# Performance work log

Hardware: AMD Instinct MI355X
Metric: run time of the kernel (lower is better)

Reference implementation:

```python
import jax, jax.numpy as jnp
import numpy as np

DEPTH = 18                 # tree levels (complete binary tree, heap layout)
N = 2**DEPTH - 1           # 262143 nodes
X_SIZE = 128
H_SIZE = 128
VOCAB = 32000


def setup_inputs() -> dict:
    key = jax.random.key(0)
    ks = jax.random.split(key, 8)
    g = lambda k, shp, sc: jax.random.normal(k, shp, dtype=jnp.float32) * sc
    return {
        "x": jax.random.randint(ks[0], (N,), 0, VOCAB, dtype=jnp.int32),
        "mask": jax.random.randint(ks[1], (N,), 0, 2, dtype=jnp.int32),
        "E": g(ks[2], (VOCAB, X_SIZE), 0.02),
        "W_iou": g(ks[3], (X_SIZE, 3 * H_SIZE), X_SIZE ** -0.5),
        "b_iou_x": jnp.zeros((3 * H_SIZE,), jnp.float32),
        "W_f": g(ks[4], (X_SIZE, H_SIZE), X_SIZE ** -0.5),
        "b_f_x": jnp.zeros((H_SIZE,), jnp.float32),
        "U_iou": g(ks[5], (H_SIZE, 3 * H_SIZE), H_SIZE ** -0.5),
        "b_iou_h": jnp.zeros((3 * H_SIZE,), jnp.float32),
        "U_f": g(ks[6], (H_SIZE, H_SIZE), H_SIZE ** -0.5),
        "b_f_h": jnp.zeros((H_SIZE,), jnp.float32),
    }


def reference(x, mask, E, W_iou, b_iou_x, W_f, b_f_x, U_iou, b_iou_h, U_f, b_f_h):
    # input_module: embedding lookup of masked token ids
    m = mask.astype(jnp.float32)[:, None]                      # [N,1]
    embeds = E[x * mask]                                       # [N,X]
    iou_in = (embeds @ W_iou + b_iou_x) * m                    # [N,3H] gated per node
    f_in = (embeds @ W_f + b_f_x) * m                          # [N,H]

    Hd = U_f.shape[0]
    h = jnp.zeros((N, Hd), jnp.float32)
    c = jnp.zeros((N, Hd), jnp.float32)

    # topological propagation: leaves -> root (prop_nodes_topo)
    for lvl in range(DEPTH - 1, -1, -1):
        s0, e0 = 2 ** lvl - 1, 2 ** (lvl + 1) - 1              # node range at this level
        iou = iou_in[s0:e0] + b_iou_h                          # apply_node bias
        if lvl == DEPTH - 1:
            c_agg = jnp.zeros((e0 - s0, Hd), jnp.float32)      # leaves: no children
        else:
            # children of node i are 2i+1 (left) and 2i+2 (right): strided gather
            hl, hr = h[2 * s0 + 1:2 * e0:2], h[2 * s0 + 2:2 * e0 + 1:2]
            cl, cr = c[2 * s0 + 1:2 * e0:2], c[2 * s0 + 2:2 * e0 + 1:2]
            # per-child forget gates (child-sum aggregator, shared U_f)
            fl = jax.nn.sigmoid(f_in[s0:e0] + hl @ U_f + b_f_h)
            fr = jax.nn.sigmoid(f_in[s0:e0] + hr @ U_f + b_f_h)
            c_agg = fl * cl + fr * cr
            iou = iou + (hl + hr) @ U_iou
        i, o, u = jnp.split(iou, 3, axis=-1)
        c_new = jax.nn.sigmoid(i) * jnp.tanh(u) + c_agg
        h_new = jax.nn.sigmoid(o) * jnp.tanh(c_new)
        h = h.at[s0:e0].set(h_new)                             # scatter back to parents
        c = c.at[s0:e0].set(c_new)
    return h                                                   # output_module = identity
```

## Files before the change

kernel.cpp:

```cpp
#include <hip/hip_runtime.h>
#include <math.h>

typedef unsigned short u16;
typedef unsigned int u32;
typedef float f32x4 __attribute__((ext_vector_type(4)));
typedef short bfrag __attribute__((ext_vector_type(8)));

#define HS 128
#define DPLANE 4096000
#define DHB    33554304

__device__ __forceinline__ float sigf(float x) { return 1.0f / (1.0f + __expf(-x)); }
__device__ __forceinline__ float tanhfast(float x) {
    float e = __expf(2.0f * x);
    return 1.0f - 2.0f / (e + 1.0f);
}
__device__ __forceinline__ u16 f2bf(float f) {
    u32 u = __float_as_uint(f);
    return (u16)((u + 0x7FFFu + ((u >> 16) & 1u)) >> 16);
}
__device__ __forceinline__ float bf2f(u16 h) { return __uint_as_float(((u32)h) << 16); }

template<int N> __device__ __forceinline__ void waitv() {
    asm volatile("s_waitcnt vmcnt(%0)" :: "i"(N) : "memory");
}

__device__ __forceinline__ float bval_int(int k, int col,
    const float* W_iou, const float* W_f, const float* U_iou, const float* U_f)
{
    if (col < 384) {
        if (k < 128) return W_iou[k * 384 + col];
        if (k < 256) return U_iou[(k - 128) * 384 + col];
        return U_iou[(k - 256) * 384 + col];
    } else if (col < 512) {
        int cc = col - 384;
        if (k < 128) return W_f[k * 128 + cc];
        if (k < 256) return U_f[(k - 128) * 128 + cc];
        return 0.0f;
    } else {
        int cc = col - 512;
        if (k < 128) return W_f[k * 128 + cc];
        if (k < 256) return 0.0f;
        return U_f[(k - 256) * 128 + cc];
    }
}

#define TOT_INT (12 * 40 * 2 * 512)
#define TOT_LEAF (4 * 24 * 2 * 512)
#define ZBF_OFF (TOT_INT + TOT_LEAF)
#define EPL_OFF (ZBF_OFF + 128)
#define TOT_E 4096000
#define ZBP_OFF (EPL_OFF + TOT_E)
#define PREP_ALL (ZBP_OFF + 128)

__global__ __launch_bounds__(256) void prep_kernel(
    const float* __restrict__ W_iou, const float* __restrict__ W_f,
    const float* __restrict__ U_iou, const float* __restrict__ U_f,
    const float* __restrict__ E,
    u16* __restrict__ Bint, u16* __restrict__ Bleaf,
    u16* __restrict__ EH, u16* __restrict__ EL,
    u16* __restrict__ zbp, float* __restrict__ zbf)
{
    int idx = blockIdx.x * 256 + threadIdx.x;
    if (idx < TOT_INT) {
        int j8 = idx & 7, l = (idx >> 3) & 63, half = (idx >> 9) & 1;
        int rest = idx >> 10;
        int cfabs = rest % 40, kc = rest / 40;
        int wq = cfabs / 5, g = cfabs % 5;
        int j = 16 * wq + (l & 15);
        int origcol = (g < 3) ? g * 128 + j : ((g == 3) ? 384 + j : 512 + j);
        int k = kc * 32 + (l >> 4) * 8 + j8;
        float v = bval_int(k, origcol, W_iou, W_f, U_iou, U_f);
        u16 hi = f2bf(v);
        Bint[idx] = half ? f2bf(v - bf2f(hi)) : hi;
    } else if (idx < TOT_INT + TOT_LEAF) {
        int i2 = idx - TOT_INT;
        int j8 = i2 & 7, l = (i2 >> 3) & 63, half = (i2 >> 9) & 1;
        int rest = i2 >> 10;
        int cfabs = rest % 24, kc = rest / 24;
        int wq = cfabs / 3, g = cfabs % 3;
        int origcol = g * 128 + 16 * wq + (l & 15);
        int k = kc * 32 + (l >> 4) * 8 + j8;
        float v = W_iou[k * 384 + origcol];
        u16 hi = f2bf(v);
        Bleaf[i2] = half ? f2bf(v - bf2f(hi)) : hi;
    } else if (idx < EPL_OFF) {
        zbf[idx - ZBF_OFF] = 0.0f;
    } else if (idx < ZBP_OFF) {
        int i3 = idx - EPL_OFF;
        float v = E[i3];
        u16 hi = f2bf(v);
        EH[i3] = hi;
        EL[i3] = f2bf(v - bf2f(hi));
    } else if (idx < PREP_ALL) {
        zbp[idx - ZBP_OFF] = 0;
    }
}

template<int NKC, int NCFA, int NCF, int MODE>
__device__ __forceinline__ void phase_gemm(
    f32x4 (&acc)[4][NCF],
    const int* __restrict__ x, const int* __restrict__ mask,
    const u16* __restrict__ EH, const u16* __restrict__ zbp,
    const u16* __restrict__ hbH,
    const u16* __restrict__ Bg,
    u16* ldsA, const u16* ldsP,
    int n0, int lastn, int t)
{
    constexpr int NB = 2 * NCF;
    const int l = t & 63, wq = t >> 6;
    const int lr = l & 15, lg = l >> 4;

    const u16 *ebp, *hb1p = nullptr, *hb2p = nullptr;
    {
        const int prow = t & 63, pk8 = ((t >> 6) & 3) * 8, pp = t >> 8;
        int ns = n0 + prow; if (ns >= lastn) ns = n0;
        const u16* Ep = pp ? (EH + DPLANE) : EH;
        ebp = (mask[ns] ? Ep + (size_t)x[ns] * HS : zbp) + pk8;
        if (MODE == 1) {
            const u16* hbp = pp ? (hbH + DHB) : hbH;
            hb1p = hbp + (size_t)(2 * ns + 1) * HS + pk8;
            hb2p = hbp + (size_t)(2 * ns + 2) * HS + pk8;
        }
    }
    auto stageA = [&](int kc, int buf) {
        const u16* src;
        if (MODE == 1) {
            int seg = kc >> 2, ks = kc & 3;
            src = (seg == 0 ? ebp : (seg == 1 ? hb1p : hb2p)) + ks * 32;
        } else {
            src = ebp + (kc & 3) * 32;
        }
        __builtin_amdgcn_global_load_lds(
            (const __attribute__((address_space(1))) void*)src,
            (__attribute__((address_space(3))) void*)(ldsA + buf * 4096 + t * 8), 16, 0, 0);
    };
    const u16* bbase = Bg + (size_t)(wq * NCF) * 1024 + (size_t)l * 8;
    auto loadB = [&](int kc, bfrag (&bh)[NCF], bfrag (&bl)[NCF]) {
        const u16* bp = bbase + (size_t)kc * ((size_t)NCFA * 1024);
#pragma unroll
        for (int cf = 0; cf < NCF; ++cf) {
            bh[cf] = *(const bfrag*)(bp + (size_t)cf * 1024);
            bl[cf] = *(const bfrag*)(bp + (size_t)cf * 1024 + 512);
        }
    };
    auto compute = [&](int kk, bfrag (&bh)[NCF], bfrag (&bl)[NCF]) {
        bfrag ah[4], al[4];
        if (MODE == 2 && kk >= 4) {
            const int seg = (kk - 4) >> 2;
            const int kk8 = ((kk - 4) & 3) * 4 + lg;
#pragma unroll
            for (int rf = 0; rf < 4; ++rf) {
                int arow = 16 * rf + lr;
                ah[rf] = *(const bfrag*)(ldsP + ((size_t)kk8 * 128 + seg * 64 + arow) * 8);
                al[rf] = *(const bfrag*)(ldsP + ((size_t)(16 + kk8) * 128 + seg * 64 + arow) * 8);
            }
        } else {
            const u16* ab = ldsA + (kk % 3) * 4096;
#pragma unroll
            for (int rf = 0; rf < 4; ++rf) {
                int arow = 16 * rf + lr;
                ah[rf] = *(const bfrag*)(ab + ((size_t)lg * 64 + arow) * 8);
                al[rf] = *(const bfrag*)(ab + ((size_t)(4 + lg) * 64 + arow) * 8);
            }
        }
#pragma unroll
        for (int cf = 0; cf < NCF; ++cf) {
#pragma unroll
            for (int rf = 0; rf < 4; ++rf)
                acc[rf][cf] = __builtin_amdgcn_mfma_f32_16x16x32_bf16(ah[rf], bh[cf], acc[rf][cf], 0, 0, 0);
#pragma unroll
            for (int rf = 0; rf < 4; ++rf)
                acc[rf][cf] = __builtin_amdgcn_mfma_f32_16x16x32_bf16(al[rf], bh[cf], acc[rf][cf], 0, 0, 0);
#pragma unroll
            for (int rf = 0; rf < 4; ++rf)
                acc[rf][cf] = __builtin_amdgcn_mfma_f32_16x16x32_bf16(ah[rf], bl[cf], acc[rf][cf], 0, 0, 0);
        }
    };

    bfrag bhA[NCF], blA[NCF], bhB[NCF], blB[NCF];
    stageA(0, 0);
    loadB(0, bhA, blA);
    stageA(1, 1);

#pragma unroll 1
    for (int kc = 0; kc < NKC; kc += 2) {
        loadB(kc + 1, bhB, blB);
        if constexpr (MODE == 2) { if (kc <= 2) waitv<NB + 1>(); else waitv<NB>(); }
        else waitv<NB + 1>();
        __builtin_amdgcn_s_barrier();
        asm volatile("" ::: "memory");
        if constexpr (MODE == 2) { if (kc + 2 < 4) stageA(kc + 2, (kc + 2) % 3); }
        else                     { if (kc + 2 <= NKC - 1) stageA(kc + 2, (kc + 2) % 3); }
        compute(kc, bhA, blA);

        { int kn = kc + 2; if (kn > NKC - 1) kn = NKC - 1; loadB(kn, bhA, blA); }
        if constexpr (MODE == 2) { if (kc == 0) waitv<NB + 1>(); else waitv<NB>(); }
        else { if (kc == NKC - 2) waitv<NB>(); else waitv<NB + 1>(); }
        __builtin_amdgcn_s_barrier();
        asm volatile("" ::: "memory");
        if constexpr (MODE == 2) { if (kc + 3 < 4) stageA(kc + 3, (kc + 3) % 3); }
        else                     { if (kc + 3 <= NKC - 1) stageA(kc + 3, (kc + 3) % 3); }
        compute(kc + 1, bhB, blB);
    }
}

template<int NCF, bool LEAF>
__device__ __forceinline__ void child_epilogue(
    f32x4 (&acc)[4][NCF],
    const int* __restrict__ mask,
    const float* __restrict__ b_iou_x, const float* __restrict__ b_f_x,
    const float* __restrict__ b_iou_h, const float* __restrict__ b_f_h,
    float* __restrict__ h, const float* __restrict__ c,
    u16* ldsP, float* ldsC,
    int n0, int lastn, int oBase, int t)
{
    const int l = t & 63, wq = t >> 6, lr = l & 15, lg = l >> 4;
    const int j = 16 * wq + lr;
    float bix = b_iou_x[j], box = b_iou_x[HS + j], bux = b_iou_x[2 * HS + j];
    float bih = b_iou_h[j], boh = b_iou_h[HS + j], buh = b_iou_h[2 * HS + j];
    float bfx = 0.0f, bfh = 0.0f;
    if constexpr (!LEAF) { bfx = b_f_x[j]; bfh = b_f_h[j]; }
#pragma unroll
    for (int rf = 0; rf < 4; ++rf) {
#pragma unroll
        for (int r = 0; r < 4; ++r) {
            int ctr = 16 * rf + 4 * lg + r;
            int n = n0 + ctr;
            if (n >= lastn) continue;
            float m = (float)mask[n];
            float iv = acc[rf][0][r] + m * bix + bih;
            float ov = acc[rf][1][r] + m * box + boh;
            float uv = acc[rf][2][r] + m * bux + buh;
            float cn;
            if constexpr (!LEAF) {
                float fl = acc[rf][3][r] + m * bfx + bfh;
                float fr = acc[rf][4][r] + m * bfx + bfh;
                float cl = c[(size_t)(2 * n + 1) * HS + j];
                float cr = c[(size_t)(2 * n + 2) * HS + j];
                cn = sigf(iv) * tanhfast(uv) + sigf(fl) * cl + sigf(fr) * cr;
            } else {
                cn = sigf(iv) * tanhfast(uv);
            }
            float hn = sigf(ov) * tanhfast(cn);
            h[(size_t)n * HS + j] = hn;
            int o = oBase + ctr;
            int half = o & 1, slot = o >> 1;
            u16 hh = f2bf(hn);
            ldsP[((size_t)(j >> 3) * 128 + half * 64 + slot) * 8 + (j & 7)] = hh;
            ldsP[((size_t)(16 + (j >> 3)) * 128 + half * 64 + slot) * 8 + (j & 7)] = f2bf(hn - bf2f(hh));
            ldsC[o * 129 + j] = cn;
        }
    }
}

__device__ __forceinline__ void parent_epilogue(
    f32x4 (&acc)[4][5],
    const int* __restrict__ mask,
    const float* __restrict__ b_iou_x, const float* __restrict__ b_f_x,
    const float* __restrict__ b_iou_h, const float* __restrict__ b_f_h,
    float* __restrict__ h, float* __restrict__ c, u16* __restrict__ hbH,
    const float* ldsC,
    int n0, int lastn, int t)
{
    u16* hbL = hbH + DHB;
    const int l = t & 63, wq = t >> 6, lr = l & 15, lg = l >> 4;
    const int j = 16 * wq + lr;
    float bix = b_iou_x[j], box = b_iou_x[HS + j], bux = b_iou_x[2 * HS + j];
    float bih = b_iou_h[j], boh = b_iou_h[HS + j], buh = b_iou_h[2 * HS + j];
    float bfx = b_f_x[j], bfh = b_f_h[j];
#pragma unroll
    for (int rf = 0; rf < 4; ++rf) {
#pragma unroll
        for (int r = 0; r < 4; ++r) {
            int ctr = 16 * rf + 4 * lg + r;
            int n = n0 + ctr;
            if (n >= lastn) continue;
            float m = (float)mask[n];
            float iv = acc[rf][0][r] + m * bix + bih;
            float ov = acc[rf][1][r] + m * box + boh;
            float uv = acc[rf][2][r] + m * bux + buh;
            float fl = acc[rf][3][r] + m * bfx + bfh;
            float fr = acc[rf][4][r] + m * bfx + bfh;
            float cl = ldsC[(2 * ctr) * 129 + j];
            float cr = ldsC[(2 * ctr + 1) * 129 + j];
            float cn = sigf(iv) * tanhfast(uv) + sigf(fl) * cl + sigf(fr) * cr;
            float hn = sigf(ov) * tanhfast(cn);
            c[(size_t)n * HS + j] = cn;
            h[(size_t)n * HS + j] = hn;
            u16 hh = f2bf(hn);
            hbH[(size_t)n * HS + j] = hh;
            hbL[(size_t)n * HS + j] = f2bf(hn - bf2f(hh));
        }
    }
}

__device__ __forceinline__ void tail_epilogue(
    f32x4 (&acc)[4][5],
    const int* __restrict__ mask,
    const float* __restrict__ b_iou_x, const float* __restrict__ b_f_x,
    const float* __restrict__ b_iou_h, const float* __restrict__ b_f_h,
    float* __restrict__ h, float* __restrict__ c, u16* __restrict__ hbH,
    int n0, int lastn, int t)
{
    u16* hbL = hbH + DHB;
    const int l = t & 63, wq = t >> 6, lr = l & 15, lg = l >> 4;
    const int j = 16 * wq + lr;
    float bix = b_iou_x[j], box = b_iou_x[HS + j], bux = b_iou_x[2 * HS + j];
    float bih = b_iou_h[j], boh = b_iou_h[HS + j], buh = b_iou_h[2 * HS + j];
    float bfx = b_f_x[j], bfh = b_f_h[j];
#pragma unroll
    for (int rf = 0; rf < 4; ++rf) {
#pragma unroll
        for (int r = 0; r < 4; ++r) {
            int ctr = 16 * rf + 4 * lg + r;
            int n = n0 + ctr;
            if (n >= lastn) continue;
            float m = (float)mask[n];
            float iv = acc[rf][0][r] + m * bix + bih;
            float ov = acc[rf][1][r] + m * box + boh;
            float uv = acc[rf][2][r] + m * bux + buh;
            float fl = acc[rf][3][r] + m * bfx + bfh;
            float fr = acc[rf][4][r] + m * bfx + bfh;
            float cl = c[(size_t)(2 * n + 1) * HS + j];
            float cr = c[(size_t)(2 * n + 2) * HS + j];
            float cn = sigf(iv) * tanhfast(uv) + sigf(fl) * cl + sigf(fr) * cr;
            float hn = sigf(ov) * tanhfast(cn);
            c[(size_t)n * HS + j] = cn;
            h[(size_t)n * HS + j] = hn;
            u16 hh = f2bf(hn);
            hbH[(size_t)n * HS + j] = hh;
            hbL[(size_t)n * HS + j] = f2bf(hn - bf2f(hh));
        }
    }
}

template<bool LEAFCH>
__global__ __launch_bounds__(512, 2) void fused_pair(
    const int* __restrict__ x, const int* __restrict__ mask,
    const u16* __restrict__ EH, const u16* __restrict__ zbp,
    const u16* __restrict__ Bint, const u16* __restrict__ Bleaf,
    const float* __restrict__ b_iou_x, const float* __restrict__ b_f_x,
    const float* __restrict__ b_iou_h, const float* __restrict__ b_f_h,
    float* __restrict__ h, float* __restrict__ c, u16* __restrict__ hbH,
    int s0p, int Mp)
{
    __shared__ __align__(16) u16 ldsA[3 * 4096];
    __shared__ __align__(16) u16 ldsP[2 * 16 * 128 * 8];
    __shared__ __align__(16) float ldsC[128 * 129];
    const int t = threadIdx.x;
    const int p0 = s0p + blockIdx.x * 64;
    const int lastp = s0p + Mp;
    const int lastc = 2 * lastp + 1;

    constexpr int CNCF = LEAFCH ? 3 : 5;
    const f32x4 zzz = {0.0f, 0.0f, 0.0f, 0.0f};

    {
        f32x4 acc[4][CNCF];
#pragma unroll
        for (int rf = 0; rf < 4; ++rf)
#pragma unroll
            for (int cf = 0; cf < CNCF; ++cf) acc[rf][cf] = zzz;
        phase_gemm<LEAFCH ? 4 : 12, LEAFCH ? 24 : 40, CNCF, LEAFCH ? 0 : 1>(
            acc, x, mask, EH, zbp, hbH, LEAFCH ? Bleaf : Bint, ldsA, ldsP, 2 * p0 + 1, lastc, t);
        child_epilogue<CNCF, LEAFCH>(acc, mask, b_iou_x, b_f_x, b_iou_h, b_f_h,
                                     h, c, ldsP, ldsC, 2 * p0 + 1, lastc, 0, t);
    }
    __syncthreads();
    {
        f32x4 acc[4][CNCF];
#pragma unroll
        for (int rf = 0; rf < 4; ++rf)
#pragma unroll
            for (int cf = 0; cf < CNCF; ++cf) acc[rf][cf] = zzz;
        phase_gemm<LEAFCH ? 4 : 12, LEAFCH ? 24 : 40, CNCF, LEAFCH ? 0 : 1>(
            acc, x, mask, EH, zbp, hbH, LEAFCH ? Bleaf : Bint, ldsA, ldsP, 2 * p0 + 65, lastc, t);
        child_epilogue<CNCF, LEAFCH>(acc, mask, b_iou_x, b_f_x, b_iou_h, b_f_h,
                                     h, c, ldsP, ldsC, 2 * p0 + 65, lastc, 64, t);
    }
    __syncthreads();
    {
        f32x4 acc[4][5];
#pragma unroll
        for (int rf = 0; rf < 4; ++rf)
#pragma unroll
            for (int cf = 0; cf < 5; ++cf) acc[rf][cf] = zzz;
        phase_gemm<12, 40, 5, 2>(acc, x, mask, EH, zbp, hbH, Bint, ldsA, ldsP, p0, lastp, t);
        parent_epilogue(acc, mask, b_iou_x, b_f_x, b_iou_h, b_f_h,
                        h, c, hbH, ldsC, p0, lastp, t);
    }
}

#define TAIL_BLOCKS 32

__device__ __forceinline__ void grid_barrier(u32* ctr, u32 target, int t) {
    __syncthreads();
    if (t == 0) {
        __threadfence();
        __hip_atomic_fetch_add(ctr, 1u, __ATOMIC_RELEASE, __HIP_MEMORY_SCOPE_AGENT);
        while (__hip_atomic_load(ctr, __ATOMIC_ACQUIRE, __HIP_MEMORY_SCOPE_AGENT) < target)
            __builtin_amdgcn_s_sleep(4);
        __threadfence();
    }
    __syncthreads();
}

__global__ __launch_bounds__(512, 2) void tail_kernel(
    const int* __restrict__ x, const int* __restrict__ mask,
    const u16* __restrict__ EH, const u16* __restrict__ zbp,
    const u16* __restrict__ Bint,
    const float* __restrict__ b_iou_x, const float* __restrict__ b_f_x,
    const float* __restrict__ b_iou_h, const float* __restrict__ b_f_h,
    float* __restrict__ h, float* __restrict__ c, u16* __restrict__ hbH,
    u32* __restrict__ bar)
{
    __shared__ __align__(16) u16 ldsA[3 * 4096];
    const int t = threadIdx.x;
    const f32x4 zzz = {0.0f, 0.0f, 0.0f, 0.0f};

#pragma unroll 1
    for (int lvl = 11; lvl >= 0; --lvl) {
        int s0 = (1 << lvl) - 1, M = 1 << lvl;
        int nb = (M + 63) >> 6;
        if ((int)blockIdx.x < nb) {
            int n0 = s0 + blockIdx.x * 64;
            int lastn = s0 + M;
            f32x4 acc[4][5];
#pragma unroll
            for (int rf = 0; rf < 4; ++rf)
#pragma unroll
                for (int cf = 0; cf < 5; ++cf) acc[rf][cf] = zzz;
            phase_gemm<12, 40, 5, 1>(acc, x, mask, EH, zbp, hbH, Bint,
                                     ldsA, nullptr, n0, lastn, t);
            tail_epilogue(acc, mask, b_iou_x, b_f_x, b_iou_h, b_f_h,
                          h, c, hbH, n0, lastn, t);
        }
        if (lvl > 0) grid_barrier(&bar[11 - lvl], TAIL_BLOCKS, t);
    }
}

extern "C" void kernel_launch(void* const* d_in, const int* in_sizes, int n_in,
                              void* d_out, int out_size, void* d_ws, size_t ws_size,
                              hipStream_t stream)
{
    const int*   x       = (const int*)d_in[0];
    const int*   mask    = (const int*)d_in[1];
    const float* E       = (const float*)d_in[2];
    const float* W_iou   = (const float*)d_in[3];
    const float* b_iou_x = (const float*)d_in[4];
    const float* W_f     = (const float*)d_in[5];
    const float* b_f_x   = (const float*)d_in[6];
    const float* U_iou   = (const float*)d_in[7];
    const float* b_iou_h = (const float*)d_in[8];
    const float* U_f     = (const float*)d_in[9];
    const float* b_f_h   = (const float*)d_in[10];

    float* h = (float*)d_out;
    char* ws = (char*)d_ws;

    u16*   Bint  = (u16*)(ws);
    u16*   Bleaf = (u16*)(ws + 983040);
    float* zbf   = (float*)(ws + 1179648);
    u32*   bar   = (u32*)(ws + 1179648);
    u16*   EH    = (u16*)(ws + 1180160);
    u16*   EL    = (u16*)(ws + 9372160);
    u16*   zbp   = (u16*)(ws + 17564160);
    float* c     = (float*)(ws + 17564416);
    u16*   hbH   = (u16*)(ws + 151781632);

    prep_kernel<<<PREP_ALL / 256, 256, 0, stream>>>(
        W_iou, W_f, U_iou, U_f, E, Bint, Bleaf, EH, EL, zbp, zbf);

    for (int lvl = 16; lvl >= 12; lvl -= 2) {
        int s0p = (1 << lvl) - 1, Mp = 1 << lvl;
        int blocks = (Mp + 63) / 64;
        if (lvl == 16)
            fused_pair<true><<<blocks, 512, 0, stream>>>(
                x, mask, EH, zbp, Bint, Bleaf,
                b_iou_x, b_f_x, b_iou_h, b_f_h, h, c, hbH, s0p, Mp);
        else
            fused_pair<false><<<blocks, 512, 0, stream>>>(
                x, mask, EH, zbp, Bint, Bleaf,
                b_iou_x, b_f_x, b_iou_h, b_f_h, h, c, hbH, s0p, Mp);
    }

    tail_kernel<<<TAIL_BLOCKS, 512, 0, stream>>>(
        x, mask, EH, zbp, Bint,
        b_iou_x, b_f_x, b_iou_h, b_f_h, h, c, hbH, bar);
}
```

Measured before the change: 687.9 us.

## Split tail kernel by output column group with LDS-resident weight slice

The tail kernel, which handles the top 12 tree levels with grid barriers between them, now uses 40 blocks instead of 32. Each block owns one of 8 output-column groups and one of 5 row groups. Each block loads its slice of the recurrent weight matrix into LDS once, then processes 128-node tiles with a double-buffered async global-to-LDS stage of the A operand. The aim is to spread the small upper levels across more blocks and stop re-streaming weights from global memory at every level. In exchange, each tile's A operand is loaded redundantly by all 8 column-group blocks, and more blocks take part in each grid barrier.

```diff
diff --git a/kernel.cpp b/kernel.cpp
--- a/kernel.cpp
+++ b/kernel.cpp
@@ -295,46 +295,6 @@
     }
 }
 
-__device__ __forceinline__ void tail_epilogue(
-    f32x4 (&acc)[4][5],
-    const int* __restrict__ mask,
-    const float* __restrict__ b_iou_x, const float* __restrict__ b_f_x,
-    const float* __restrict__ b_iou_h, const float* __restrict__ b_f_h,
-    float* __restrict__ h, float* __restrict__ c, u16* __restrict__ hbH,
-    int n0, int lastn, int t)
-{
-    u16* hbL = hbH + DHB;
-    const int l = t & 63, wq = t >> 6, lr = l & 15, lg = l >> 4;
-    const int j = 16 * wq + lr;
-    float bix = b_iou_x[j], box = b_iou_x[HS + j], bux = b_iou_x[2 * HS + j];
-    float bih = b_iou_h[j], boh = b_iou_h[HS + j], buh = b_iou_h[2 * HS + j];
-    float bfx = b_f_x[j], bfh = b_f_h[j];
-#pragma unroll
-    for (int rf = 0; rf < 4; ++rf) {
-#pragma unroll
-        for (int r = 0; r < 4; ++r) {
-            int ctr = 16 * rf + 4 * lg + r;
-            int n = n0 + ctr;
-            if (n >= lastn) continue;
-            float m = (float)mask[n];
-            float iv = acc[rf][0][r] + m * bix + bih;
-            float ov = acc[rf][1][r] + m * box + boh;
-            float uv = acc[rf][2][r] + m * bux + buh;
-            float fl = acc[rf][3][r] + m * bfx + bfh;
-            float fr = acc[rf][4][r] + m * bfx + bfh;
-            float cl = c[(size_t)(2 * n + 1) * HS + j];
-            float cr = c[(size_t)(2 * n + 2) * HS + j];
-            float cn = sigf(iv) * tanhfast(uv) + sigf(fl) * cl + sigf(fr) * cr;
-            float hn = sigf(ov) * tanhfast(cn);
-            c[(size_t)n * HS + j] = cn;
-            h[(size_t)n * HS + j] = hn;
-            u16 hh = f2bf(hn);
-            hbH[(size_t)n * HS + j] = hh;
-            hbL[(size_t)n * HS + j] = f2bf(hn - bf2f(hh));
-        }
-    }
-}
-
 template<bool LEAFCH>
 __global__ __launch_bounds__(512, 2) void fused_pair(
     const int* __restrict__ x, const int* __restrict__ mask,
@@ -392,7 +352,7 @@
     }
 }
 
-#define TAIL_BLOCKS 32
+#define TAIL_BLOCKS 40
 
 __device__ __forceinline__ void grid_barrier(u32* ctr, u32 target, int t) {
     __syncthreads();
@@ -415,26 +375,110 @@
     float* __restrict__ h, float* __restrict__ c, u16* __restrict__ hbH,
     u32* __restrict__ bar)
 {
-    __shared__ __align__(16) u16 ldsA[3 * 4096];
+    __shared__ __align__(16) u16 ldsB[120 * 512];
+    __shared__ __align__(16) u16 ldsA[2 * 8192];
     const int t = threadIdx.x;
+    const int wq = blockIdx.x & 7;
+    const int rg = blockIdx.x >> 3;
+    const int l = t & 63, w = t >> 6;
+    const int lr = l & 15, lg = l >> 4;
+    u16* hbL = hbH + DHB;
+
+    for (int rr = 0; rr < 15; ++rr) {
+        int s = rr * 8 + w;
+        int kcq = s / 10, rem = s % 10, cf = rem >> 1, half = rem & 1;
+        const u16* src = Bint + ((size_t)((kcq * 40 + wq * 5 + cf) * 2 + half)) * 512 + l * 8;
+        *(bfrag*)(ldsB + (size_t)s * 512 + l * 8) = *(const bfrag*)src;
+    }
+    __syncthreads();
+
+    const int j = 16 * wq + lr;
+    const float bix = b_iou_x[j], box = b_iou_x[HS + j], bux = b_iou_x[2 * HS + j];
+    const float bih = b_iou_h[j], boh = b_iou_h[HS + j], buh = b_iou_h[2 * HS + j];
+    const float bfx = b_f_x[j], bfh = b_f_h[j];
+
+    const int row = t & 127, kslot = (t >> 7) & 3;
     const f32x4 zzz = {0.0f, 0.0f, 0.0f, 0.0f};
 
 #pragma unroll 1
     for (int lvl = 11; lvl >= 0; --lvl) {
-        int s0 = (1 << lvl) - 1, M = 1 << lvl;
-        int nb = (M + 63) >> 6;
-        if ((int)blockIdx.x < nb) {
-            int n0 = s0 + blockIdx.x * 64;
-            int lastn = s0 + M;
-            f32x4 acc[4][5];
-#pragma unroll
-            for (int rf = 0; rf < 4; ++rf)
-#pragma unroll
-                for (int cf = 0; cf < 5; ++cf) acc[rf][cf] = zzz;
-            phase_gemm<12, 40, 5, 1>(acc, x, mask, EH, zbp, hbH, Bint,
-                                     ldsA, nullptr, n0, lastn, t);
-            tail_epilogue(acc, mask, b_iou_x, b_f_x, b_iou_h, b_f_h,
-                          h, c, hbH, n0, lastn, t);
+        const int s0 = (1 << lvl) - 1, M = 1 << lvl;
+        const int lastn = s0 + M;
+        const int ntiles = (M + 127) >> 7;
+#pragma unroll 1
+        for (int tile = rg; tile < ntiles; tile += 5) {
+            const int n0 = s0 + tile * 128;
+            int ns = n0 + row; if (ns >= lastn) ns = n0;
+            const int mk = mask[ns];
+            const u16* pE = (mk ? EH + (size_t)x[ns] * HS : zbp) + kslot * 8;
+            const int dE = mk ? DPLANE : 0;
+            const u16* p1 = hbH + (size_t)(2 * ns + 1) * HS + kslot * 8;
+            const u16* p2 = hbH + (size_t)(2 * ns + 2) * HS + kslot * 8;
+
+            auto stageA = [&](int kc, int buf) {
+                const u16 *sh; int dd;
+                int ks = kc & 3;
+                if (kc < 4)      { sh = pE + ks * 32; dd = dE; }
+                else if (kc < 8) { sh = p1 + ks * 32; dd = DHB; }
+                else             { sh = p2 + ks * 32; dd = DHB; }
+                u16* d = ldsA + buf * 8192 + t * 8;
+                __builtin_amdgcn_global_load_lds(
+                    (const __attribute__((address_space(1))) void*)sh,
+                    (__attribute__((address_space(3))) void*)d, 16, 0, 0);
+                __builtin_amdgcn_global_load_lds(
+                    (const __attribute__((address_space(1))) void*)(sh + dd),
+                    (__attribute__((address_space(3))) void*)(d + 4096), 16, 0, 0);
+            };
+
+            f32x4 acc[5];
+#pragma unroll
+            for (int cf = 0; cf < 5; ++cf) acc[cf] = zzz;
+
+            stageA(0, 0);
+            stageA(1, 1);
+#pragma unroll 1
+            for (int kc = 0; kc < 12; ++kc) {
+                if (kc < 11) waitv<2>(); else waitv<0>();
+                __builtin_amdgcn_s_barrier();
+                asm volatile("" ::: "memory");
+                const u16* ab = ldsA + (kc & 1) * 8192;
+                const int arow = 16 * w + lr;
+                bfrag ah = *(const bfrag*)(ab + ((size_t)lg * 128 + arow) * 8);
+                bfrag al = *(const bfrag*)(ab + ((size_t)(512 + lg * 128 + arow)) * 8);
+                const u16* bb = ldsB + (size_t)kc * (10 * 512) + l * 8;
+#pragma unroll
+                for (int cf = 0; cf < 5; ++cf) {
+                    bfrag bh = *(const bfrag*)(bb + (size_t)(2 * cf) * 512);
+                    bfrag bl = *(const bfrag*)(bb + (size_t)(2 * cf + 1) * 512);
+                    acc[cf] = __builtin_amdgcn_mfma_f32_16x16x32_bf16(ah, bh, acc[cf], 0, 0, 0);
+                    acc[cf] = __builtin_amdgcn_mfma_f32_16x16x32_bf16(al, bh, acc[cf], 0, 0, 0);
+                    acc[cf] = __builtin_amdgcn_mfma_f32_16x16x32_bf16(ah, bl, acc[cf], 0, 0, 0);
+                }
+                __builtin_amdgcn_s_barrier();
+                asm volatile("" ::: "memory");
+                if (kc + 2 < 12) stageA(kc + 2, kc & 1);
+            }
+
+#pragma unroll
+            for (int r = 0; r < 4; ++r) {
+                int n = n0 + 16 * w + 4 * lg + r;
+                if (n >= lastn) continue;
+                float m = (float)mask[n];
+                float iv = acc[0][r] + m * bix + bih;
+                float ov = acc[1][r] + m * box + boh;
+                float uv = acc[2][r] + m * bux + buh;
+                float fl = acc[3][r] + m * bfx + bfh;
+                float fr = acc[4][r] + m * bfx + bfh;
+                float cl = c[(size_t)(2 * n + 1) * HS + j];
+                float cr = c[(size_t)(2 * n + 2) * HS + j];
+                float cn = sigf(iv) * tanhfast(uv) + sigf(fl) * cl + sigf(fr) * cr;
+                float hn = sigf(ov) * tanhfast(cn);
+                c[(size_t)n * HS + j] = cn;
+                h[(size_t)n * HS + j] = hn;
+                u16 hh = f2bf(hn);
+                hbH[(size_t)n * HS + j] = hh;
+                hbL[(size_t)n * HS + j] = f2bf(hn - bf2f(hh));
+            }
         }
         if (lvl > 0) grid_barrier(&bar[11 - lvl], TAIL_BLOCKS, t);
     }
```

New measurement: 619.9 us. 9.9% less time.
